# Performance work log

Hardware: AMD Instinct MI355X
Metric: run time of the kernel (lower is better)

## Reference

```python
import jax
import jax.numpy as jnp
import numpy as np

# Module configuration (matches init_kwargs)
N, C, H, W = 8, 256, 64, 64
CO, KH, KW = 256, 3, 3
SH, SW = 1, 1
PH, PW = 1, 1
DH, DW = 1, 1
G, DG = 1, 1
K = KH * KW
HO = (H + 2 * PH - (DH * (KH - 1) + 1)) // SH + 1
WO = (W + 2 * PW - (DW * (KW - 1) + 1)) // SW + 1


def setup_inputs() -> dict:
    key = jax.random.key(0)
    k1, k2, k3, k4 = jax.random.split(key, 4)
    x = jax.random.normal(k1, (N, C, H, W), dtype=jnp.float32)
    offset = jax.random.normal(k2, (N, DG * 2 * K, HO, WO), dtype=jnp.float32)
    mask = jax.random.uniform(k3, (N, DG * K, HO, WO), dtype=jnp.float32)
    stdv = 1.0 / np.sqrt(C * KH * KW)
    weight = jax.random.uniform(k4, (CO, C // G, KH, KW), dtype=jnp.float32,
                                minval=-stdv, maxval=stdv)
    return {"x": x, "offset": offset, "mask": mask, "weight": weight}


def _deform_sample(x, offset, mask):
    """Modulated deformable bilinear sampling (DCNv2 im2col).

    Returns columns [N, C, K, HO, WO].
    """
    Cg = C // DG
    # offset layout: [N, DG, K, 2(y,x), HO, WO]
    off = offset.reshape(N, DG, K, 2, HO, WO)
    off_y, off_x = off[:, :, :, 0], off[:, :, :, 1]

    # Base sampling grid per kernel tap: [K, HO, WO] broadcastable
    kgy = (jnp.repeat(jnp.arange(KH), KW) * DH).astype(jnp.float32)  # [K]
    kgx = (jnp.tile(jnp.arange(KW), KH) * DW).astype(jnp.float32)    # [K]
    oy = (jnp.arange(HO) * SH - PH).astype(jnp.float32)              # [HO]
    ox = (jnp.arange(WO) * SW - PW).astype(jnp.float32)              # [WO]
    py = kgy[:, None, None] + oy[None, :, None] + off_y  # [N,DG,K,HO,WO]
    px = kgx[:, None, None] + ox[None, None, :] + off_x  # [N,DG,K,HO,WO]

    y0 = jnp.floor(py)
    x0 = jnp.floor(px)
    ly = py - y0
    lx = px - x0
    y0i = y0.astype(jnp.int32)
    x0i = x0.astype(jnp.int32)
    y1i = y0i + 1
    x1i = x0i + 1

    xf = x.reshape(N, DG, Cg, H * W)

    def gather_one(xf_nd, idx_nd):
        # xf_nd: [Cg, H*W], idx_nd: [K*HO*WO] -> [Cg, K*HO*WO]
        return xf_nd[:, idx_nd]

    gather = jax.vmap(jax.vmap(gather_one))  # over N, DG

    def corner(yi, xi, wgt):
        valid = (yi >= 0) & (yi < H) & (xi >= 0) & (xi < W)
        yc = jnp.clip(yi, 0, H - 1)
        xc = jnp.clip(xi, 0, W - 1)
        idx = (yc * W + xc).reshape(N, DG, K * HO * WO)
        g = gather(xf, idx).reshape(N, DG, Cg, K, HO, WO)
        w = (wgt * valid.astype(x.dtype))[:, :, None]  # [N,DG,1,K,HO,WO]
        return g * w

    cols = corner(y0i, x0i, (1.0 - ly) * (1.0 - lx))
    cols = cols + corner(y0i, x1i, (1.0 - ly) * lx)
    cols = cols + corner(y1i, x0i, ly * (1.0 - lx))
    cols = cols + corner(y1i, x1i, ly * lx)

    # modulation
    m = mask.reshape(N, DG, 1, K, HO, WO)
    cols = cols * m
    return cols.reshape(N, C, K, HO, WO)


def reference(x, offset, mask, weight):
    cols = _deform_sample(x, offset, mask)              # [N,C,K,HO,WO]
    colsg = cols.reshape(N, G, C // G, K, HO, WO)
    wg = weight.reshape(G, CO // G, C // G, K)
    out = jnp.einsum('ngckhw,gock->ngohw', colsg, wg)
    return out.reshape(N, CO, HO, WO)
```

## Files before the change

### kernel.cpp

```cpp
#include <hip/hip_runtime.h>
#include <hip/hip_bf16.h>
#include <hip/hip_fp16.h>
#include <stdint.h>

#define N_   8
#define C_   256
#define H_   64
#define W_   64
#define CO_  256
#define K_   9
#define HO_  64
#define WO_  64
#define CK_  (C_ * K_)
#define P_   (HO_ * WO_)

#define BN   128
#define BK   64
#define NT   36
#define NTHR 1024

typedef __attribute__((ext_vector_type(8))) _Float16 f16x8;
typedef __attribute__((ext_vector_type(4))) float f32x4;

__device__ __forceinline__ unsigned short f2bf(float f) {
    uint32_t u = __builtin_bit_cast(uint32_t, f);
    uint32_t r = (u + 0x7FFFu + ((u >> 16) & 1u)) >> 16;
    return (unsigned short)r;
}
__device__ __forceinline__ float bf2f(unsigned short u) {
    return __builtin_bit_cast(float, (uint32_t)u << 16);
}
__device__ __forceinline__ unsigned short f2h(float f) {
    return __builtin_bit_cast(unsigned short, (_Float16)f);
}


__global__ __launch_bounds__(256)
void transpose_x(const float* __restrict__ x, unsigned short* __restrict__ xT) {
    __shared__ float t[64][65];
    const int n  = blockIdx.z;
    const int c0 = blockIdx.y * 64;
    const int h0 = blockIdx.x * 64;
    const int tx = threadIdx.x & 63;
    const int ty = threadIdx.x >> 6;
    const float* xp = x + ((size_t)n * C_ + c0) * P_ + h0;
    #pragma unroll
    for (int i = 0; i < 16; ++i) {
        int c = ty * 16 + i;
        t[c][tx] = xp[(size_t)c * P_ + tx];
    }
    __syncthreads();
    unsigned short* op = xT + ((size_t)n * P_ + h0) * C_ + c0;
    #pragma unroll
    for (int i = 0; i < 16; ++i) {
        int hw = ty * 16 + i;
        op[(size_t)hw * C_ + tx] = f2h(t[tx][hw]);
    }
}

__global__ __launch_bounds__(256)
void reorder_w(const float* __restrict__ w, unsigned short* __restrict__ Wt) {
    const int co = blockIdx.x;
    const int c  = threadIdx.x;
    const float* src = w + (size_t)co * CK_ + (size_t)c * K_;
    float v[9];
    #pragma unroll
    for (int k = 0; k < 9; ++k) v[k] = src[k];
    #pragma unroll
    for (int k = 0; k < 9; ++k)
        Wt[(size_t)co * CK_ + k * C_ + c] = f2h(v[k]);
}

__device__ __forceinline__ void barrier_lgkm_only() {
    __builtin_amdgcn_sched_barrier(0);
    asm volatile("s_waitcnt lgkmcnt(0)" ::: "memory");
    __builtin_amdgcn_s_barrier();
    __builtin_amdgcn_sched_barrier(0);
}

#define COMB(dst, A, B, Cc, D) do {                                   \
    __half2 _v = __hmul2(W0, __builtin_bit_cast(__half2, (A)));       \
    _v = __hfma2(W1, __builtin_bit_cast(__half2, (B)), _v);           \
    _v = __hfma2(W2, __builtin_bit_cast(__half2, (Cc)), _v);          \
    _v = __hfma2(W3, __builtin_bit_cast(__half2, (D)), _v);           \
    (dst) = __builtin_bit_cast(unsigned, _v); } while (0)

__global__ __launch_bounds__(NTHR, 4)
void dcn_main(const unsigned short* __restrict__ xT,
              const unsigned short* __restrict__ Wt,
              const float* __restrict__ offset,
              const float* __restrict__ mask,
              float* __restrict__ out) {
    __shared__ uint2 sIdx[BN * K_];
    __shared__ uint4 sWd [BN * K_];
    __shared__ unsigned short sWs[2][CO_ * BK];
    __shared__ unsigned short sBs[2][BN * BK];

    const int tid = threadIdx.x;
    const int bid = blockIdx.x;
    const int n   = bid & 7;
    const int p0  = (bid >> 3) * BN;

    for (int e = tid; e < BN * K_; e += NTHR) {
        int pl = e / K_;
        int k  = e - pl * K_;
        int p  = p0 + pl;
        int ho = p >> 6, wo = p & 63;
        float offy = offset[(size_t)((n * 2 * K_ + 2 * k)     * P_) + p];
        float offx = offset[(size_t)((n * 2 * K_ + 2 * k + 1) * P_) + p];
        float m    = mask  [(size_t)((n * K_ + k) * P_) + p];
        float py = (float)(k / 3 + ho - 1) + offy;
        float px = (float)(k % 3 + wo - 1) + offx;
        float y0f = floorf(py), x0f = floorf(px);
        float ly = py - y0f,   lx = px - x0f;
        int y0 = (int)y0f, x0 = (int)x0f;
        int y1 = y0 + 1,   x1 = x0 + 1;
        bool vy0 = (y0 >= 0) & (y0 < H_);
        bool vy1 = (y1 >= 0) & (y1 < H_);
        bool vx0 = (x0 >= 0) & (x0 < W_);
        bool vx1 = (x1 >= 0) & (x1 < W_);
        float w00 = (1.f - ly) * (1.f - lx) * m * ((vy0 & vx0) ? 1.f : 0.f);
        float w01 = (1.f - ly) * lx         * m * ((vy0 & vx1) ? 1.f : 0.f);
        float w10 = ly * (1.f - lx)         * m * ((vy1 & vx0) ? 1.f : 0.f);
        float w11 = ly * lx                 * m * ((vy1 & vx1) ? 1.f : 0.f);
        unsigned int cy0 = (unsigned)min(max(y0, 0), H_ - 1);
        unsigned int cy1 = (unsigned)min(max(y1, 0), H_ - 1);
        unsigned int cx0 = (unsigned)min(max(x0, 0), W_ - 1);
        unsigned int cx1 = (unsigned)min(max(x1, 0), W_ - 1);
        sIdx[e] = make_uint2((cy0 * W_ + cx0) | ((cy0 * W_ + cx1) << 16),
                             (cy1 * W_ + cx0) | ((cy1 * W_ + cx1) << 16));
        sWd[e] = make_uint4((unsigned)f2h(w00) * 0x10001u,
                            (unsigned)f2h(w01) * 0x10001u,
                            (unsigned)f2h(w10) * 0x10001u,
                            (unsigned)f2h(w11) * 0x10001u);
    }
    __syncthreads();

    const unsigned short* xTn = xT + (size_t)n * P_ * C_;

    const int spl = tid >> 3;
    const int cs  = tid & 7;
    const int boff = spl * 128 + ((cs ^ (spl & 7)) << 4);
    const int wco  = tid >> 2;
    const int wsl  = tid & 3;
    const int wswz = wco & 7;
    const int woff = wco * 128;
    const unsigned short* wsrcbase = Wt + (size_t)wco * CK_ + wsl * 8;

    const int lane = tid & 63;
    const int wid  = tid >> 6;
    const int wm   = (wid & 7) * 32;
    const int wp   = (wid >> 3) * 64;
    const int l15  = lane & 15;
    const int l4   = lane >> 4;
    const int slA  = l4 ^ (l15 & 7);

    f32x4 acc[2][4] = {};

    uint4 qa, qb, qc, qd;
    uint4 wq0, wq1;

#define PREF(TT) {                                                        \
        const int kn  = (TT) >> 2;                                        \
        const int c0n = ((TT) & 3) * 64;                                  \
        const unsigned short* ws = wsrcbase + kn * C_ + c0n;              \
        wq0 = *(const uint4*)(ws);                                        \
        wq1 = *(const uint4*)(ws + 32);                                   \
        uint2 id = sIdx[spl * K_ + kn];                                   \
        const unsigned short* base = xTn + c0n + cs * 8;                  \
        qa = *(const uint4*)(base + ((size_t)(id.x & 0xFFFFu) << 8));     \
        qb = *(const uint4*)(base + ((size_t)(id.x >> 16)     << 8));     \
        qc = *(const uint4*)(base + ((size_t)(id.y & 0xFFFFu) << 8));     \
        qd = *(const uint4*)(base + ((size_t)(id.y >> 16)     << 8));     \
    }

#define STAGE(TT, WB, BB) {                                               \
        char* wrB = (char*)(WB) + woff;                                   \
        *(uint4*)(wrB + ((wsl       ^ wswz) << 4)) = wq0;                 \
        *(uint4*)(wrB + (((wsl + 4) ^ wswz) << 4)) = wq1;                 \
        uint4 wv = sWd[spl * K_ + ((TT) >> 2)];                           \
        __half2 W0 = __builtin_bit_cast(__half2, wv.x);                   \
        __half2 W1 = __builtin_bit_cast(__half2, wv.y);                   \
        __half2 W2 = __builtin_bit_cast(__half2, wv.z);                   \
        __half2 W3 = __builtin_bit_cast(__half2, wv.w);                   \
        uint4 r;                                                          \
        COMB(r.x, qa.x, qb.x, qc.x, qd.x);                                \
        COMB(r.y, qa.y, qb.y, qc.y, qd.y);                                \
        COMB(r.z, qa.z, qb.z, qc.z, qd.z);                                \
        COMB(r.w, qa.w, qb.w, qc.w, qd.w);                                \
        *(uint4*)((char*)(BB) + boff) = r;                                \
    }

    PREF(0)
    STAGE(0, sWs[0], sBs[0])
    PREF(1)

    for (int t = 0; t < NT; ++t) {
        const int br = t & 1;
        const char* wR = (const char*)sWs[br];
        const char* bR = (const char*)sBs[br];

        barrier_lgkm_only();

        f16x8 A0, A1, B0, B1, B2, B3;
        {
            const int sl = slA;
            B0 = *(const f16x8*)(bR + (wp      + l15) * 128 + (sl << 4));
            B1 = *(const f16x8*)(bR + (wp + 16 + l15) * 128 + (sl << 4));
            B2 = *(const f16x8*)(bR + (wp + 32 + l15) * 128 + (sl << 4));
            B3 = *(const f16x8*)(bR + (wp + 48 + l15) * 128 + (sl << 4));
            A0 = *(const f16x8*)(wR + (wm      + l15) * 128 + (sl << 4));
            A1 = *(const f16x8*)(wR + (wm + 16 + l15) * 128 + (sl << 4));
        }

        if (t + 1 < NT) {
            if (br) { STAGE(t + 1, sWs[0], sBs[0]) }
            else    { STAGE(t + 1, sWs[1], sBs[1]) }
            if (t + 2 < NT) PREF(t + 2)
        }

        acc[0][0] = __builtin_amdgcn_mfma_f32_16x16x32_f16(A0, B0, acc[0][0], 0, 0, 0);
        acc[0][1] = __builtin_amdgcn_mfma_f32_16x16x32_f16(A0, B1, acc[0][1], 0, 0, 0);
        acc[0][2] = __builtin_amdgcn_mfma_f32_16x16x32_f16(A0, B2, acc[0][2], 0, 0, 0);
        acc[0][3] = __builtin_amdgcn_mfma_f32_16x16x32_f16(A0, B3, acc[0][3], 0, 0, 0);
        acc[1][0] = __builtin_amdgcn_mfma_f32_16x16x32_f16(A1, B0, acc[1][0], 0, 0, 0);
        acc[1][1] = __builtin_amdgcn_mfma_f32_16x16x32_f16(A1, B1, acc[1][1], 0, 0, 0);
        acc[1][2] = __builtin_amdgcn_mfma_f32_16x16x32_f16(A1, B2, acc[1][2], 0, 0, 0);
        acc[1][3] = __builtin_amdgcn_mfma_f32_16x16x32_f16(A1, B3, acc[1][3], 0, 0, 0);

        {
            const int sl = slA ^ 4;
            B0 = *(const f16x8*)(bR + (wp      + l15) * 128 + (sl << 4));
            B1 = *(const f16x8*)(bR + (wp + 16 + l15) * 128 + (sl << 4));
            B2 = *(const f16x8*)(bR + (wp + 32 + l15) * 128 + (sl << 4));
            B3 = *(const f16x8*)(bR + (wp + 48 + l15) * 128 + (sl << 4));
            A0 = *(const f16x8*)(wR + (wm      + l15) * 128 + (sl << 4));
            A1 = *(const f16x8*)(wR + (wm + 16 + l15) * 128 + (sl << 4));
        }
        acc[0][0] = __builtin_amdgcn_mfma_f32_16x16x32_f16(A0, B0, acc[0][0], 0, 0, 0);
        acc[0][1] = __builtin_amdgcn_mfma_f32_16x16x32_f16(A0, B1, acc[0][1], 0, 0, 0);
        acc[0][2] = __builtin_amdgcn_mfma_f32_16x16x32_f16(A0, B2, acc[0][2], 0, 0, 0);
        acc[0][3] = __builtin_amdgcn_mfma_f32_16x16x32_f16(A0, B3, acc[0][3], 0, 0, 0);
        acc[1][0] = __builtin_amdgcn_mfma_f32_16x16x32_f16(A1, B0, acc[1][0], 0, 0, 0);
        acc[1][1] = __builtin_amdgcn_mfma_f32_16x16x32_f16(A1, B1, acc[1][1], 0, 0, 0);
        acc[1][2] = __builtin_amdgcn_mfma_f32_16x16x32_f16(A1, B2, acc[1][2], 0, 0, 0);
        acc[1][3] = __builtin_amdgcn_mfma_f32_16x16x32_f16(A1, B3, acc[1][3], 0, 0, 0);
    }
#undef PREF
#undef STAGE

    float* outn = out + (size_t)n * CO_ * P_;
    #pragma unroll
    for (int m = 0; m < 2; ++m) {
        int co = wm + m * 16 + l4 * 4;
        #pragma unroll
        for (int nn = 0; nn < 4; ++nn) {
            int p = p0 + wp + nn * 16 + l15;
            #pragma unroll
            for (int r = 0; r < 4; ++r) {
                outn[(size_t)(co + r) * P_ + p] = acc[m][nn][r];
            }
        }
    }
}

template <int TAG>
__global__ __launch_bounds__(512, 2)
void dcn_fb(const float* __restrict__ x,
            const float* __restrict__ offset,
            const float* __restrict__ mask,
            const float* __restrict__ weight,
            float* __restrict__ out) {
    typedef __attribute__((ext_vector_type(8))) short bf16x8;
    __shared__ uint2  sIdx[128 * K_];
    __shared__ float4 sW  [128 * K_];
    __shared__ unsigned short sWs[CO_ * 32];
    __shared__ unsigned short sBs[128 * 32];

    const int tid = threadIdx.x;
    const int n  = blockIdx.y;
    const int p0 = blockIdx.x * 128;

    for (int e = tid; e < 128 * K_; e += 512) {
        int pl = e / K_;
        int k  = e - pl * K_;
        int p  = p0 + pl;
        int ho = p >> 6, wo = p & 63;
        float offy = offset[(size_t)((n * 2 * K_ + 2 * k)     * P_) + p];
        float offx = offset[(size_t)((n * 2 * K_ + 2 * k + 1) * P_) + p];
        float m    = mask  [(size_t)((n * K_ + k) * P_) + p];
        float py = (float)(k / 3 + ho - 1) + offy;
        float px = (float)(k % 3 + wo - 1) + offx;
        float y0f = floorf(py), x0f = floorf(px);
        float ly = py - y0f,   lx = px - x0f;
        int y0 = (int)y0f, x0 = (int)x0f;
        int y1 = y0 + 1,   x1 = x0 + 1;
        bool vy0 = (y0 >= 0) & (y0 < H_);
        bool vy1 = (y1 >= 0) & (y1 < H_);
        bool vx0 = (x0 >= 0) & (x0 < W_);
        bool vx1 = (x1 >= 0) & (x1 < W_);
        float w00 = (1.f - ly) * (1.f - lx) * m * ((vy0 & vx0) ? 1.f : 0.f);
        float w01 = (1.f - ly) * lx         * m * ((vy0 & vx1) ? 1.f : 0.f);
        float w10 = ly * (1.f - lx)         * m * ((vy1 & vx0) ? 1.f : 0.f);
        float w11 = ly * lx                 * m * ((vy1 & vx1) ? 1.f : 0.f);
        unsigned int cy0 = (unsigned)min(max(y0, 0), H_ - 1);
        unsigned int cy1 = (unsigned)min(max(y1, 0), H_ - 1);
        unsigned int cx0 = (unsigned)min(max(x0, 0), W_ - 1);
        unsigned int cx1 = (unsigned)min(max(x1, 0), W_ - 1);
        sIdx[e] = make_uint2((cy0 * W_ + cx0) | ((cy0 * W_ + cx1) << 16),
                             (cy1 * W_ + cx0) | ((cy1 * W_ + cx1) << 16));
        sW[e]   = make_float4(w00, w01, w10, w11);
    }

    const float* xn = x + (size_t)n * C_ * P_;
    const int pl   = tid >> 2;
    const int pl9  = pl * K_;
    const int ckb  = (tid & 3) * 8;
    const int wco  = tid >> 1;
    const int wck  = (tid & 1) * 16;

    const int lane = tid & 63;
    const int wid  = tid >> 6;
    const int wm   = (wid & 1) * 128;
    const int wp   = (wid >> 1) * 32;
    const int l15  = lane & 15;
    const int l4   = lane >> 4;

    f32x4 acc[8][2] = {};

    for (int ck0 = 0; ck0 < CK_; ck0 += 32) {
        __syncthreads();
        {
            const float4* wsrc = (const float4*)(weight + (size_t)wco * CK_ + ck0 + wck);
            float4 wa = wsrc[0], wb = wsrc[1], wc = wsrc[2], wd = wsrc[3];
            uint4 q0, q1;
            q0.x = f2bf(wa.x) | ((unsigned)f2bf(wa.y) << 16);
            q0.y = f2bf(wa.z) | ((unsigned)f2bf(wa.w) << 16);
            q0.z = f2bf(wb.x) | ((unsigned)f2bf(wb.y) << 16);
            q0.w = f2bf(wb.z) | ((unsigned)f2bf(wb.w) << 16);
            q1.x = f2bf(wc.x) | ((unsigned)f2bf(wc.y) << 16);
            q1.y = f2bf(wc.z) | ((unsigned)f2bf(wc.w) << 16);
            q1.z = f2bf(wd.x) | ((unsigned)f2bf(wd.y) << 16);
            q1.w = f2bf(wd.z) | ((unsigned)f2bf(wd.w) << 16);
            *(uint4*)&sWs[wco * 32 + wck]     = q0;
            *(uint4*)&sWs[wco * 32 + wck + 8] = q1;
        }
        {
            int ckstart = ck0 + ckb;
            int cc = ckstart / 9;
            int kk = ckstart - cc * 9;
            unsigned int packed[4];
            unsigned short colv[8];
            #pragma unroll
            for (int j = 0; j < 8; ++j) {
                int e = pl9 + kk;
                uint2  id = sIdx[e];
                float4 wv = sW[e];
                const float* xp = xn + ((size_t)cc << 12);
                float v = wv.x * xp[id.x & 0xFFFFu]
                        + wv.y * xp[id.x >> 16]
                        + wv.z * xp[id.y & 0xFFFFu]
                        + wv.w * xp[id.y >> 16];
                colv[j] = f2bf(v);
                ++kk; if (kk == 9) { kk = 0; ++cc; }
            }
            packed[0] = colv[0] | ((unsigned)colv[1] << 16);
            packed[1] = colv[2] | ((unsigned)colv[3] << 16);
            packed[2] = colv[4] | ((unsigned)colv[5] << 16);
            packed[3] = colv[6] | ((unsigned)colv[7] << 16);
            *(uint4*)&sBs[pl * 32 + ckb] = *(uint4*)packed;
        }
        __syncthreads();
        bf16x8 bfr0 = *(const bf16x8*)&sBs[(wp + l15)      * 32 + l4 * 8];
        bf16x8 bfr1 = *(const bf16x8*)&sBs[(wp + 16 + l15) * 32 + l4 * 8];
        #pragma unroll
        for (int m = 0; m < 8; ++m) {
            bf16x8 afr = *(const bf16x8*)&sWs[(wm + m * 16 + l15) * 32 + l4 * 8];
            acc[m][0] = __builtin_amdgcn_mfma_f32_16x16x32_bf16(afr, bfr0, acc[m][0], 0, 0, 0);
            acc[m][1] = __builtin_amdgcn_mfma_f32_16x16x32_bf16(afr, bfr1, acc[m][1], 0, 0, 0);
        }
    }

    float* outn = out + (size_t)n * CO_ * P_;
    #pragma unroll
    for (int m = 0; m < 8; ++m) {
        int co = wm + m * 16 + l4 * 4;
        #pragma unroll
        for (int nn = 0; nn < 2; ++nn) {
            int p = p0 + wp + nn * 16 + l15;
            #pragma unroll
            for (int r = 0; r < 4; ++r) {
                outn[(size_t)(co + r) * P_ + p] = acc[m][nn][r];
            }
        }
    }
}

extern "C" void kernel_launch(void* const* d_in, const int* in_sizes, int n_in,
                              void* d_out, int out_size, void* d_ws, size_t ws_size,
                              hipStream_t stream) {
    const float* x      = (const float*)d_in[0];
    const float* offset = (const float*)d_in[1];
    const float* mask   = (const float*)d_in[2];
    const float* weight = (const float*)d_in[3];
    float* out = (float*)d_out;

    const size_t xT_elems = (size_t)N_ * P_ * C_;
    const size_t Wt_elems = (size_t)CO_ * CK_;
    const size_t need     = (xT_elems + Wt_elems) * sizeof(unsigned short);

    if (ws_size >= need) {
        unsigned short* xT = (unsigned short*)d_ws;
        unsigned short* Wt = xT + xT_elems;
        transpose_x<<<dim3(P_ / 64, C_ / 64, N_), dim3(256), 0, stream>>>(x, xT);
        reorder_w<<<dim3(CO_), dim3(256), 0, stream>>>(weight, Wt);
        dcn_main<<<dim3((P_ / BN) * N_), dim3(NTHR), 0, stream>>>(xT, Wt, offset, mask, out);
    } else if (ws_size >= (8u << 20)) {
        dcn_fb<1><<<dim3(P_ / 128, N_), dim3(512), 0, stream>>>(x, offset, mask, weight, out);
    } else {
        dcn_fb<0><<<dim3(P_ / 128, N_), dim3(512), 0, stream>>>(x, offset, mask, weight, out);
    }
}
```

Before: 68.97 us.

## Split K-dimension across two wave groups with 64x64 warp tiles and LDS reduction

Reorganizes the 16 waves into two groups that each handle half of the 64-wide K slice (one 32-wide MFMA step each), with every wave computing a 64x64 output tile instead of 32x64. This cuts redundant LDS fragment loads per MFMA (more reuse of each A and B fragment). The partial sums are combined through shared memory at the end with extra barriers. It doubles the accumulator registers per wave, which may pressure occupancy under the launch bounds.

```diff
diff --git a/kernel.cpp b/kernel.cpp
--- a/kernel.cpp
+++ b/kernel.cpp
@@ -149,13 +149,15 @@
 
     const int lane = tid & 63;
     const int wid  = tid >> 6;
-    const int wm   = (wid & 7) * 32;
-    const int wp   = (wid >> 3) * 64;
+    const int g    = wid >> 3;
+    const int w8   = wid & 7;
+    const int wm4  = (w8 & 3) * 64;
+    const int wp2  = (w8 >> 2) * 64;
     const int l15  = lane & 15;
     const int l4   = lane >> 4;
-    const int slA  = l4 ^ (l15 & 7);
-
-    f32x4 acc[2][4] = {};
+    const int slG  = (l4 ^ (l15 & 7)) ^ (g << 2);
+
+    f32x4 acc[4][4] = {};
 
     uint4 qa, qb, qc, qd;
     uint4 wq0, wq1;
@@ -202,16 +204,10 @@
 
         barrier_lgkm_only();
 
-        f16x8 A0, A1, B0, B1, B2, B3;
-        {
-            const int sl = slA;
-            B0 = *(const f16x8*)(bR + (wp      + l15) * 128 + (sl << 4));
-            B1 = *(const f16x8*)(bR + (wp + 16 + l15) * 128 + (sl << 4));
-            B2 = *(const f16x8*)(bR + (wp + 32 + l15) * 128 + (sl << 4));
-            B3 = *(const f16x8*)(bR + (wp + 48 + l15) * 128 + (sl << 4));
-            A0 = *(const f16x8*)(wR + (wm      + l15) * 128 + (sl << 4));
-            A1 = *(const f16x8*)(wR + (wm + 16 + l15) * 128 + (sl << 4));
-        }
+        f16x8 B0 = *(const f16x8*)(bR + (wp2      + l15) * 128 + (slG << 4));
+        f16x8 B1 = *(const f16x8*)(bR + (wp2 + 16 + l15) * 128 + (slG << 4));
+        f16x8 B2 = *(const f16x8*)(bR + (wp2 + 32 + l15) * 128 + (slG << 4));
+        f16x8 B3 = *(const f16x8*)(bR + (wp2 + 48 + l15) * 128 + (slG << 4));
 
         if (t + 1 < NT) {
             if (br) { STAGE(t + 1, sWs[0], sBs[0]) }
@@ -219,46 +215,50 @@
             if (t + 2 < NT) PREF(t + 2)
         }
 
-        acc[0][0] = __builtin_amdgcn_mfma_f32_16x16x32_f16(A0, B0, acc[0][0], 0, 0, 0);
-        acc[0][1] = __builtin_amdgcn_mfma_f32_16x16x32_f16(A0, B1, acc[0][1], 0, 0, 0);
-        acc[0][2] = __builtin_amdgcn_mfma_f32_16x16x32_f16(A0, B2, acc[0][2], 0, 0, 0);
-        acc[0][3] = __builtin_amdgcn_mfma_f32_16x16x32_f16(A0, B3, acc[0][3], 0, 0, 0);
-        acc[1][0] = __builtin_amdgcn_mfma_f32_16x16x32_f16(A1, B0, acc[1][0], 0, 0, 0);
-        acc[1][1] = __builtin_amdgcn_mfma_f32_16x16x32_f16(A1, B1, acc[1][1], 0, 0, 0);
-        acc[1][2] = __builtin_amdgcn_mfma_f32_16x16x32_f16(A1, B2, acc[1][2], 0, 0, 0);
-        acc[1][3] = __builtin_amdgcn_mfma_f32_16x16x32_f16(A1, B3, acc[1][3], 0, 0, 0);
-
-        {
-            const int sl = slA ^ 4;
-            B0 = *(const f16x8*)(bR + (wp      + l15) * 128 + (sl << 4));
-            B1 = *(const f16x8*)(bR + (wp + 16 + l15) * 128 + (sl << 4));
-            B2 = *(const f16x8*)(bR + (wp + 32 + l15) * 128 + (sl << 4));
-            B3 = *(const f16x8*)(bR + (wp + 48 + l15) * 128 + (sl << 4));
-            A0 = *(const f16x8*)(wR + (wm      + l15) * 128 + (sl << 4));
-            A1 = *(const f16x8*)(wR + (wm + 16 + l15) * 128 + (sl << 4));
-        }
-        acc[0][0] = __builtin_amdgcn_mfma_f32_16x16x32_f16(A0, B0, acc[0][0], 0, 0, 0);
-        acc[0][1] = __builtin_amdgcn_mfma_f32_16x16x32_f16(A0, B1, acc[0][1], 0, 0, 0);
-        acc[0][2] = __builtin_amdgcn_mfma_f32_16x16x32_f16(A0, B2, acc[0][2], 0, 0, 0);
-        acc[0][3] = __builtin_amdgcn_mfma_f32_16x16x32_f16(A0, B3, acc[0][3], 0, 0, 0);
-        acc[1][0] = __builtin_amdgcn_mfma_f32_16x16x32_f16(A1, B0, acc[1][0], 0, 0, 0);
-        acc[1][1] = __builtin_amdgcn_mfma_f32_16x16x32_f16(A1, B1, acc[1][1], 0, 0, 0);
-        acc[1][2] = __builtin_amdgcn_mfma_f32_16x16x32_f16(A1, B2, acc[1][2], 0, 0, 0);
-        acc[1][3] = __builtin_amdgcn_mfma_f32_16x16x32_f16(A1, B3, acc[1][3], 0, 0, 0);
+        #pragma unroll
+        for (int mf = 0; mf < 4; ++mf) {
+            f16x8 A = *(const f16x8*)(wR + (wm4 + mf * 16 + l15) * 128 + (slG << 4));
+            acc[mf][0] = __builtin_amdgcn_mfma_f32_16x16x32_f16(A, B0, acc[mf][0], 0, 0, 0);
+            acc[mf][1] = __builtin_amdgcn_mfma_f32_16x16x32_f16(A, B1, acc[mf][1], 0, 0, 0);
+            acc[mf][2] = __builtin_amdgcn_mfma_f32_16x16x32_f16(A, B2, acc[mf][2], 0, 0, 0);
+            acc[mf][3] = __builtin_amdgcn_mfma_f32_16x16x32_f16(A, B3, acc[mf][3], 0, 0, 0);
+        }
     }
 #undef PREF
 #undef STAGE
 
-    float* outn = out + (size_t)n * CO_ * P_;
-    #pragma unroll
-    for (int m = 0; m < 2; ++m) {
-        int co = wm + m * 16 + l4 * 4;
+    f32x4* red = (f32x4*)sWs;
+    const int ridx = (w8 * 64 + lane) * 4;
+    #pragma unroll
+    for (int mf = 0; mf < 4; ++mf) {
+        __syncthreads();
+        if (g == 1) {
+            red[ridx + 0] = acc[mf][0];
+            red[ridx + 1] = acc[mf][1];
+            red[ridx + 2] = acc[mf][2];
+            red[ridx + 3] = acc[mf][3];
+        }
+        __syncthreads();
+        if (g == 0) {
+            acc[mf][0] += red[ridx + 0];
+            acc[mf][1] += red[ridx + 1];
+            acc[mf][2] += red[ridx + 2];
+            acc[mf][3] += red[ridx + 3];
+        }
+    }
+
+    if (g == 0) {
+        float* outn = out + (size_t)n * CO_ * P_;
         #pragma unroll
-        for (int nn = 0; nn < 4; ++nn) {
-            int p = p0 + wp + nn * 16 + l15;
+        for (int mf = 0; mf < 4; ++mf) {
+            int co = wm4 + mf * 16 + l4 * 4;
             #pragma unroll
-            for (int r = 0; r < 4; ++r) {
-                outn[(size_t)(co + r) * P_ + p] = acc[m][nn][r];
+            for (int nn = 0; nn < 4; ++nn) {
+                int p = p0 + wp2 + nn * 16 + l15;
+                #pragma unroll
+                for (int r = 0; r < 4; ++r) {
+                    outn[(size_t)(co + r) * P_ + p] = acc[mf][nn][r];
+                }
             }
         }
     }
```

New measurement: 71.46 us. 1.04x slower.
